# Kernel tuning notes

Measured on AMD Instinct MI355X. Metric: run time of the kernel, lower is better.

The kernel has to match this reference:

```python
import jax, jax.numpy as jnp
import numpy as np

S, B, D, H, F = 2048, 2, 1024, 16, 4096
HD = D // H
EPS = 1e-5


def setup_inputs() -> dict:
    key = jax.random.key(0)
    ks = jax.random.split(key, 16)
    sc_d = 1.0 / np.sqrt(D)
    sc_f = 1.0 / np.sqrt(F)
    return {
        "src": jax.random.normal(ks[0], (S, B, D), jnp.float32),
        # attention projections: Linear weights stored as [in, out] (y = x @ W + b)
        "Wq": jax.random.normal(ks[1], (D, D), jnp.float32) * sc_d,
        "bq": jnp.zeros((D,), jnp.float32),
        "Wk": jax.random.normal(ks[2], (D, D), jnp.float32) * sc_d,
        "bk": jnp.zeros((D,), jnp.float32),
        "Wv": jax.random.normal(ks[3], (D, D), jnp.float32) * sc_d,
        "bv": jnp.zeros((D,), jnp.float32),
        "Wo": jax.random.normal(ks[4], (D, D), jnp.float32) * sc_d,
        "bo": jnp.zeros((D,), jnp.float32),
        # norm1
        "g1": jnp.ones((D,), jnp.float32),
        "be1": jnp.zeros((D,), jnp.float32),
        # FFN
        "W1": jax.random.normal(ks[5], (D, F), jnp.float32) * sc_d,
        "bf1": jnp.zeros((F,), jnp.float32),
        "W2": jax.random.normal(ks[6], (F, D), jnp.float32) * sc_f,
        "bf2": jnp.zeros((D,), jnp.float32),
        # norm2
        "g2": jnp.ones((D,), jnp.float32),
        "be2": jnp.zeros((D,), jnp.float32),
    }


def _layernorm(x, g, b):
    m = jnp.mean(x, axis=-1, keepdims=True)
    v = jnp.mean(jnp.square(x - m), axis=-1, keepdims=True)
    return (x - m) * jax.lax.rsqrt(v + EPS) * g + b


def reference(src, Wq, bq, Wk, bk, Wv, bv, Wo, bo, g1, be1, W1, bf1, W2, bf2, g2, be2):
    # --- self attention (dropout_p=0 / eval mode => dropouts are identity) ---
    scaling = float(HD) ** -0.5
    q = (src @ Wq + bq) * scaling            # [S,B,D]
    k = src @ Wk + bk
    v = src @ Wv + bv
    # split heads: torch view(S, B*H, hd) == reshape(S, B, H, hd)
    qh = q.reshape(S, B, H, HD)
    kh = k.reshape(S, B, H, HD)
    vh = v.reshape(S, B, H, HD)
    scores = jnp.einsum("sbhd,tbhd->bhst", qh, kh)      # [B,H,S,S]
    attn = jax.nn.softmax(scores, axis=-1)
    ctx = jnp.einsum("bhst,tbhd->sbhd", attn, vh).reshape(S, B, D)
    attn_out = ctx @ Wo + bo
    # residual + norm1
    x = _layernorm(src + attn_out, g1, be1)
    # FFN (ReLU)
    ff = jax.nn.relu(x @ W1 + bf1) @ W2 + bf2
    # residual + norm2
    return _layernorm(x + ff, g2, be2)
```

## Files before the change

### kernel.cpp

```cpp
#include <hip/hip_runtime.h>
#include <hip/hip_bf16.h>

#define S_  2048
#define B_  2
#define D_  1024
#define H_  16
#define F_  4096
#define HD_ 64
#define NT_ (S_*B_)

typedef __attribute__((ext_vector_type(8))) short short8;
typedef __attribute__((ext_vector_type(4))) short short4v;
typedef __attribute__((ext_vector_type(4))) float f32x4;

#define MFMA16x16x32(a,b,c) __builtin_amdgcn_mfma_f32_16x16x32_bf16((a),(b),(c),0,0,0)

#define AS1C(p) ((const __attribute__((address_space(1))) void*)(p))
#define AS3(p)  ((__attribute__((address_space(3))) void*)(p))

__device__ __forceinline__ short f2b(float f) {
  union { float f; unsigned u; } x; x.f = f;
  unsigned r = x.u + 0x7FFFu + ((x.u >> 16) & 1u);
  return (short)(r >> 16);
}
__device__ __forceinline__ float b2f(short u) {
  union { unsigned u; float f; } x; x.u = ((unsigned)(unsigned short)u) << 16;
  return x.f;
}
__device__ __forceinline__ unsigned cvtpk(float a, float b) {
  unsigned r;
  asm("v_cvt_pk_bf16_f32 %0, %1, %2" : "=v"(r) : "v"(a), "v"(b));
  return r;
}
__device__ __forceinline__ float exp2fast(float x) {
  float r;
  asm("v_exp_f32 %0, %1" : "=v"(r) : "v"(x));
  return r;
}

__global__ __launch_bounds__(256) void prep_k(
    const float* __restrict__ src, short* __restrict__ xb,
    const float* __restrict__ Wq, const float* __restrict__ Wk,
    const float* __restrict__ Wv, const float* __restrict__ Wo,
    const float* __restrict__ W1, const float* __restrict__ W2,
    short* __restrict__ Wqkv_t, short* __restrict__ Wo_t,
    short* __restrict__ W1_t, short* __restrict__ W2_t) {
  __shared__ short t[32][33];
  int bid = blockIdx.x;
  if (bid < 2048) {
    int i = (bid * 256 + threadIdx.x) * 8;
    float4 a = *(const float4*)(src + i);
    float4 b = *(const float4*)(src + i + 4);
    short8 o;
    o[0] = f2b(a.x); o[1] = f2b(a.y); o[2] = f2b(a.z); o[3] = f2b(a.w);
    o[4] = f2b(b.x); o[5] = f2b(b.y); o[6] = f2b(b.z); o[7] = f2b(b.w);
    *(short8*)(xb + i) = o;
    return;
  }
  bid -= 2048;
  const float* W; short* Wt; int N, colbase, outK, bx, by;
  if (bid < 4096) {
    int which = bid >> 10, loc = bid & 1023;
    bx = loc & 31; by = loc >> 5;
    N = 1024; outK = 1024;
    if (which == 0)      { W = Wq; Wt = Wqkv_t; colbase = 0; }
    else if (which == 1) { W = Wk; Wt = Wqkv_t; colbase = 1024; }
    else if (which == 2) { W = Wv; Wt = Wqkv_t; colbase = 2048; }
    else                 { W = Wo; Wt = Wo_t;   colbase = 0; }
  } else if (bid < 8192) {
    int loc = bid - 4096;
    bx = loc & 127; by = loc >> 7;
    W = W1; Wt = W1_t; N = 4096; colbase = 0; outK = 1024;
  } else {
    int loc = bid - 8192;
    bx = loc & 31; by = loc >> 5;
    W = W2; Wt = W2_t; N = 1024; colbase = 0; outK = 4096;
  }
  int tx = threadIdx.x & 31, ty = threadIdx.x >> 5;
  int kbase = by * 32, nbase = bx * 32;
#pragma unroll
  for (int yy = 0; yy < 4; ++yy) {
    int kk = ty + yy * 8;
    t[kk][tx] = f2b(W[(size_t)(kbase + kk) * N + nbase + tx]);
  }
  __syncthreads();
#pragma unroll
  for (int yy = 0; yy < 4; ++yy) {
    int nn = ty + yy * 8;
    Wt[(size_t)(nbase + nn + colbase) * outK + kbase + tx] = t[tx][nn];
  }
}

template<int MODE>
__global__ __launch_bounds__(256, 2) void gemm_bt(
    const short* __restrict__ A, const short* __restrict__ Bt,
    int M, int N, int K, int lda,
    const float* __restrict__ bias0, const float* __restrict__ bias1,
    const float* __restrict__ bias2,
    float* __restrict__ outf,
    short* __restrict__ outq, short* __restrict__ outk, short* __restrict__ outv) {
  __shared__ __align__(16) short As[128 * 64];
  __shared__ __align__(16) short Bs[128 * 64];
  int tid = threadIdx.x;
  int lane = tid & 63, w = tid >> 6;
  int g = lane >> 4, r = lane & 15;
  int wm = w >> 1, wn = w & 1;

  int gx = gridDim.x, gy = gridDim.y;
  int nwg = gx * gy * gridDim.z;
  int flat = (blockIdx.z * gy + blockIdx.y) * gx + blockIdx.x;
  int cpx = nwg >> 3;
  int swz = (flat & 7) * cpx + (flat >> 3);
  int z = swz / (gx * gy);
  int rem = swz - z * gx * gy;
  int row0 = (rem / gx) * 128;
  int col0 = (rem % gx) * 128;
  size_t koff = (size_t)z * K;

  f32x4 acc[4][4];
#pragma unroll
  for (int m = 0; m < 4; ++m)
#pragma unroll
    for (int n = 0; n < 4; ++n) acc[m][n] = (f32x4){0.f, 0.f, 0.f, 0.f};

  for (int kt = 0; kt < K; kt += 64) {
#pragma unroll
    for (int p = 0; p < 4; ++p) {
      int idx = tid + p * 256;
      int row = idx >> 3, c = idx & 7;
      int scol = ((c ^ (row & 7)) << 3);
      __builtin_amdgcn_global_load_lds(AS1C(A  + (size_t)(row0 + row) * lda + koff + kt + scol),
                                       AS3(As + idx * 8), 16, 0, 0);
      __builtin_amdgcn_global_load_lds(AS1C(Bt + (size_t)(col0 + row) * lda + koff + kt + scol),
                                       AS3(Bs + idx * 8), 16, 0, 0);
    }
    __syncthreads();
    short8 af[4][2], bfr[4][2];
#pragma unroll
    for (int m = 0; m < 4; ++m)
#pragma unroll
      for (int kk = 0; kk < 2; ++kk) {
        int row = wm * 64 + m * 16 + r;
        af[m][kk] = *(const short8*)(As + row * 64 + (((kk * 4 + g) ^ (r & 7)) << 3));
      }
#pragma unroll
    for (int n = 0; n < 4; ++n)
#pragma unroll
      for (int kk = 0; kk < 2; ++kk) {
        int row = wn * 64 + n * 16 + r;
        bfr[n][kk] = *(const short8*)(Bs + row * 64 + (((kk * 4 + g) ^ (r & 7)) << 3));
      }
#pragma unroll
    for (int m = 0; m < 4; ++m)
#pragma unroll
      for (int n = 0; n < 4; ++n)
#pragma unroll
        for (int kk = 0; kk < 2; ++kk)
          acc[m][n] = MFMA16x16x32(af[m][kk], bfr[n][kk], acc[m][n]);
    __syncthreads();
  }

  int rb = row0 + wm * 64, cb = col0 + wn * 64;
#pragma unroll
  for (int m = 0; m < 4; ++m) {
#pragma unroll
    for (int n = 0; n < 4; ++n) {
#pragma unroll
      for (int j = 0; j < 4; ++j) {
        int row = rb + m * 16 + g * 4 + j;
        int col = cb + n * 16 + r;
        float v = acc[m][n][j];
        if (MODE == 0) {
          int s = row >> 1, b = row & 1;
          if (col < 1024) {
            float q = (v + bias0[col]) * (0.125f * 1.44269504088896f);
            int h = col >> 6, hd = col & 63;
            outq[((size_t)(b * H_ + h) * S_ + s) * HD_ + hd] = f2b(q);
          } else if (col < 2048) {
            int c2 = col - 1024;
            float kk = v + bias1[c2];
            int h = c2 >> 6, hd = c2 & 63;
            outk[((size_t)(b * H_ + h) * S_ + s) * HD_ + hd] = f2b(kk);
          } else {
            int c2 = col - 2048;
            float vv = v + bias2[c2];
            int h = c2 >> 6, hd = c2 & 63;
            outv[((size_t)(b * H_ + h) * HD_ + hd) * S_ + s] = f2b(vv);
          }
        } else if (MODE == 2) {
          size_t o = (size_t)row * N + col;
          float t = v + bias0[col];
          outq[o] = f2b(t > 0.f ? t : 0.f);
        } else {
          outf[(size_t)z * M * N + (size_t)row * N + col] = v;
        }
      }
    }
  }
}

__global__ __launch_bounds__(256, 4) void flash_attn(const short* __restrict__ Q,
                                                     const short* __restrict__ Kb,
                                                     const short* __restrict__ Vt,
                                                     short* __restrict__ ctx) {
  __shared__ __align__(16) short Ks[2][64 * 64];
  __shared__ __align__(16) short Vs[2][64 * 64];
  __shared__ __align__(16) short P[4][16][64];
  int tid = threadIdx.x;
  int lane = tid & 63, w = tid >> 6;
  int g = lane >> 4, r = lane & 15;
  int f = blockIdx.x;
  int xcd = f & 7, loc = f >> 3;
  int bh = xcd * 4 + (loc >> 5);
  int qt = loc & 31;
  const short* qp = Q  + (size_t)bh * S_ * HD_;
  const short* kp = Kb + (size_t)bh * S_ * HD_;
  const short* vp = Vt + (size_t)bh * HD_ * S_;
  int q0 = qt * 64 + w * 16;

  short8 qf[2];
#pragma unroll
  for (int kk = 0; kk < 2; ++kk)
    qf[kk] = *(const short8*)(qp + (size_t)(q0 + r) * HD_ + kk * 32 + g * 8);

  f32x4 acc[4];
  float mi = -1e30f, li = 0.f;
#pragma unroll
  for (int db = 0; db < 4; ++db) acc[db] = (f32x4){0.f, 0.f, 0.f, 0.f};

#pragma unroll
  for (int p = 0; p < 2; ++p) {
    int idx = tid + p * 256;
    int row = idx >> 3, c = idx & 7;
    int scol = ((c ^ (row & 7)) << 3);
    __builtin_amdgcn_global_load_lds(AS1C(kp + (size_t)row * HD_ + scol),
                                     AS3(&Ks[0][0] + idx * 8), 16, 0, 0);
    __builtin_amdgcn_global_load_lds(AS1C(vp + (size_t)row * S_ + scol),
                                     AS3(&Vs[0][0] + idx * 8), 16, 0, 0);
  }
  __syncthreads();

  int cur = 0;
  for (int t = 0; t < S_ / 64; ++t) {
    if (t + 1 < S_ / 64) {
      int kv1 = (t + 1) * 64;
#pragma unroll
      for (int p = 0; p < 2; ++p) {
        int idx = tid + p * 256;
        int row = idx >> 3, c = idx & 7;
        int scol = ((c ^ (row & 7)) << 3);
        __builtin_amdgcn_global_load_lds(AS1C(kp + (size_t)(kv1 + row) * HD_ + scol),
                                         AS3(&Ks[cur ^ 1][0] + idx * 8), 16, 0, 0);
        __builtin_amdgcn_global_load_lds(AS1C(vp + (size_t)row * S_ + kv1 + scol),
                                         AS3(&Vs[cur ^ 1][0] + idx * 8), 16, 0, 0);
      }
    }
    const short* Kc = &Ks[cur][0];
    const short* Vc = &Vs[cur][0];
    short8 kf[4][2];
#pragma unroll
    for (int kb = 0; kb < 4; ++kb)
#pragma unroll
      for (int kk = 0; kk < 2; ++kk) {
        int row = kb * 16 + r;
        kf[kb][kk] = *(const short8*)(Kc + row * 64 + (((kk * 4 + g) ^ (r & 7)) << 3));
      }

    f32x4 st[4];
    __builtin_amdgcn_s_setprio(1);
#pragma unroll
    for (int kb = 0; kb < 4; ++kb) {
      f32x4 tt = (f32x4){0.f, 0.f, 0.f, 0.f};
      tt = MFMA16x16x32(kf[kb][0], qf[0], tt);
      tt = MFMA16x16x32(kf[kb][1], qf[1], tt);
      st[kb] = tt;
    }
    __builtin_amdgcn_s_setprio(0);

    float t0 = fmaxf(fmaxf(st[0][0], st[0][1]), fmaxf(st[0][2], st[0][3]));
    float t1 = fmaxf(fmaxf(st[1][0], st[1][1]), fmaxf(st[1][2], st[1][3]));
    float t2 = fmaxf(fmaxf(st[2][0], st[2][1]), fmaxf(st[2][2], st[2][3]));
    float t3 = fmaxf(fmaxf(st[3][0], st[3][1]), fmaxf(st[3][2], st[3][3]));
    float pm = fmaxf(fmaxf(t0, t1), fmaxf(t2, t3));
    if (!__all(pm <= mi + 8.0f)) {
      pm = fmaxf(pm, __shfl_xor(pm, 16));
      pm = fmaxf(pm, __shfl_xor(pm, 32));
      float mn = fmaxf(mi, pm);
      float sc2 = exp2fast(mi - mn);
      mi = mn;
      li *= sc2;
#pragma unroll
      for (int db = 0; db < 4; ++db)
#pragma unroll
        for (int j = 0; j < 4; ++j) acc[db][j] *= sc2;
    }
    float rp[4];
#pragma unroll
    for (int kb = 0; kb < 4; ++kb) {
#pragma unroll
      for (int j = 0; j < 4; ++j) st[kb][j] = exp2fast(st[kb][j] - mi);
      rp[kb] = (st[kb][0] + st[kb][1]) + (st[kb][2] + st[kb][3]);
    }
    li += (rp[0] + rp[1]) + (rp[2] + rp[3]);

#pragma unroll
    for (int kb = 0; kb < 4; ++kb) {
      unsigned w0 = cvtpk(st[kb][0], st[kb][1]);
      unsigned w1 = cvtpk(st[kb][2], st[kb][3]);
      unsigned long long pw = (unsigned long long)w0 | ((unsigned long long)w1 << 32);
      int col = (kb * 16 + g * 4) ^ ((r & 7) << 3);
      *(unsigned long long*)(&P[w][r][0] + col) = pw;
    }

    short8 vf[4][2];
#pragma unroll
    for (int db = 0; db < 4; ++db)
#pragma unroll
      for (int ks = 0; ks < 2; ++ks) {
        int row = db * 16 + r;
        vf[db][ks] = *(const short8*)(Vc + row * 64 + (((ks * 4 + g) ^ (r & 7)) << 3));
      }
    short8 pf[2];
#pragma unroll
    for (int ks = 0; ks < 2; ++ks) {
      int col = (ks * 32 + g * 8) ^ ((r & 7) << 3);
      pf[ks] = *(const short8*)(&P[w][r][0] + col);
    }

    __builtin_amdgcn_s_setprio(1);
#pragma unroll
    for (int db = 0; db < 4; ++db) {
      acc[db] = MFMA16x16x32(vf[db][0], pf[0], acc[db]);
      acc[db] = MFMA16x16x32(vf[db][1], pf[1], acc[db]);
    }
    __builtin_amdgcn_s_setprio(0);

    __syncthreads();
    cur ^= 1;
  }

  li += __shfl_xor(li, 16);
  li += __shfl_xor(li, 32);

  int b = bh >> 4, h = bh & 15;
  float inv = 1.0f / li;
  int s = q0 + r;
  int token = s * B_ + b;
#pragma unroll
  for (int db = 0; db < 4; ++db) {
    unsigned w0 = cvtpk(acc[db][0] * inv, acc[db][1] * inv);
    unsigned w1 = cvtpk(acc[db][2] * inv, acc[db][3] * inv);
    unsigned long long pw = (unsigned long long)w0 | ((unsigned long long)w1 << 32);
    *(unsigned long long*)(ctx + (size_t)token * D_ + h * 64 + db * 16 + g * 4) = pw;
  }
}

template<int RESBF16, int WF, int WB>
__global__ __launch_bounds__(256) void layernorm_fused(
    const float* __restrict__ p0, const float* __restrict__ p1,
    const float* __restrict__ bias,
    const float* __restrict__ residf, const short* __restrict__ residb,
    const float* __restrict__ gm, const float* __restrict__ bt,
    float* __restrict__ of, short* __restrict__ ob) {
  __shared__ float r1[4], r2[4];
  int row = blockIdx.x, tid = threadIdx.x;
  size_t base = (size_t)row * D_ + tid * 4;
  float4 a = *(const float4*)(p0 + base);
  float4 b = *(const float4*)(p1 + base);
  float4 bi = *(const float4*)(bias + tid * 4);
  float4 v;
  if (RESBF16) {
    short4v rb = *(const short4v*)(residb + base);
    v.x = a.x + b.x + bi.x + b2f(rb[0]);
    v.y = a.y + b.y + bi.y + b2f(rb[1]);
    v.z = a.z + b.z + bi.z + b2f(rb[2]);
    v.w = a.w + b.w + bi.w + b2f(rb[3]);
  } else {
    float4 rf = *(const float4*)(residf + base);
    v.x = a.x + b.x + bi.x + rf.x;
    v.y = a.y + b.y + bi.y + rf.y;
    v.z = a.z + b.z + bi.z + rf.z;
    v.w = a.w + b.w + bi.w + rf.w;
  }
  float s1 = v.x + v.y + v.z + v.w;
  float s2 = v.x * v.x + v.y * v.y + v.z * v.z + v.w * v.w;
#pragma unroll
  for (int off = 32; off > 0; off >>= 1) {
    s1 += __shfl_xor(s1, off, 64);
    s2 += __shfl_xor(s2, off, 64);
  }
  int wid = tid >> 6;
  if ((tid & 63) == 0) { r1[wid] = s1; r2[wid] = s2; }
  __syncthreads();
  s1 = r1[0] + r1[1] + r1[2] + r1[3];
  s2 = r2[0] + r2[1] + r2[2] + r2[3];
  float mean = s1 * (1.0f / D_);
  float var = s2 * (1.0f / D_) - mean * mean;
  float rstd = rsqrtf(var + 1e-5f);
  float4 gv = *(const float4*)(gm + tid * 4);
  float4 bv = *(const float4*)(bt + tid * 4);
  float o0 = (v.x - mean) * rstd * gv.x + bv.x;
  float o1 = (v.y - mean) * rstd * gv.y + bv.y;
  float o2 = (v.z - mean) * rstd * gv.z + bv.z;
  float o3 = (v.w - mean) * rstd * gv.w + bv.w;
  if (WF) *(float4*)(of + base) = make_float4(o0, o1, o2, o3);
  if (WB) {
    short4v o;
    o[0] = f2b(o0); o[1] = f2b(o1); o[2] = f2b(o2); o[3] = f2b(o3);
    *(short4v*)(ob + base) = o;
  }
}

extern "C" void kernel_launch(void* const* d_in, const int* in_sizes, int n_in,
                              void* d_out, int out_size, void* d_ws, size_t ws_size,
                              hipStream_t stream) {
  const float* src = (const float*)d_in[0];
  const float* Wq  = (const float*)d_in[1];
  const float* bq  = (const float*)d_in[2];
  const float* Wk  = (const float*)d_in[3];
  const float* bk  = (const float*)d_in[4];
  const float* Wv  = (const float*)d_in[5];
  const float* bv  = (const float*)d_in[6];
  const float* Wo  = (const float*)d_in[7];
  const float* bo  = (const float*)d_in[8];
  const float* g1  = (const float*)d_in[9];
  const float* be1 = (const float*)d_in[10];
  const float* W1  = (const float*)d_in[11];
  const float* bf1 = (const float*)d_in[12];
  const float* W2  = (const float*)d_in[13];
  const float* bf2 = (const float*)d_in[14];
  const float* g2  = (const float*)d_in[15];
  const float* be2 = (const float*)d_in[16];
  float* out = (float*)d_out;
  char* ws = (char*)d_ws;

  const size_t MiB = 1024 * 1024;
  short* Wqkv_t = (short*)(ws + 0 * MiB);
  short* Wo_t   = (short*)(ws + 6 * MiB);
  short* W1_t   = (short*)(ws + 8 * MiB);
  short* W2_t   = (short*)(ws + 16 * MiB);
  short* xb     = (short*)(ws + 24 * MiB);
  short* x1b    = (short*)(ws + 24 * MiB);
  short* ctx    = (short*)(ws + 32 * MiB);
  short* qb_    = (short*)(ws + 40 * MiB);
  short* kb_    = (short*)(ws + 48 * MiB);
  short* vb_    = (short*)(ws + 56 * MiB);
  short* hid    = (short*)(ws + 32 * MiB);
  float* part   = (float*)(ws + 64 * MiB);
  float* part1  = part + (size_t)NT_ * D_;

  prep_k<<<14336, 256, 0, stream>>>(src, xb, Wq, Wk, Wv, Wo, W1, W2,
                                    Wqkv_t, Wo_t, W1_t, W2_t);

  gemm_bt<0><<<dim3(24, 32, 1), 256, 0, stream>>>(xb, Wqkv_t, NT_, 3072, 1024, 1024,
                                                  bq, bk, bv, nullptr, qb_, kb_, vb_);
  flash_attn<<<1024, 256, 0, stream>>>(qb_, kb_, vb_, ctx);
  gemm_bt<3><<<dim3(8, 32, 2), 256, 0, stream>>>(ctx, Wo_t, NT_, 1024, 512, 1024,
                                                 nullptr, nullptr, nullptr, part,
                                                 nullptr, nullptr, nullptr);
  layernorm_fused<0, 0, 1><<<NT_, 256, 0, stream>>>(part, part1, bo, src, nullptr,
                                                    g1, be1, nullptr, x1b);
  gemm_bt<2><<<dim3(32, 32, 1), 256, 0, stream>>>(x1b, W1_t, NT_, 4096, 1024, 1024,
                                                  bf1, nullptr, nullptr, nullptr,
                                                  hid, nullptr, nullptr);
  gemm_bt<3><<<dim3(8, 32, 2), 256, 0, stream>>>(hid, W2_t, NT_, 1024, 2048, 4096,
                                                 nullptr, nullptr, nullptr, part,
                                                 nullptr, nullptr, nullptr);
  layernorm_fused<1, 1, 0><<<NT_, 256, 0, stream>>>(part, part1, bf2, nullptr, x1b,
                                                    g2, be2, out, nullptr);
}
```

Measured before the change: 226.4 us.

## Give each flash-attention wave two query fragments and halve the block to 128 threads

The flash attention kernel now runs 2 waves per block instead of 4, and each wave handles 32 query rows as two 16-row fragments. Each K/V fragment read from shared memory then feeds twice as many MFMAs, which cuts LDS traffic per FLOP. Each thread also issues more of the global-to-LDS staging loads. The cost is roughly double the accumulator and score registers per wave, and fewer waves per block to hide latency, which may lower occupancy.

New measurement: 226.1 us. About the same (-0.1%).

```diff
diff --git a/kernel.cpp b/kernel.cpp
--- a/kernel.cpp
+++ b/kernel.cpp
@@ -199,13 +199,13 @@
   }
 }
 
-__global__ __launch_bounds__(256, 4) void flash_attn(const short* __restrict__ Q,
+__global__ __launch_bounds__(128, 2) void flash_attn(const short* __restrict__ Q,
                                                      const short* __restrict__ Kb,
                                                      const short* __restrict__ Vt,
                                                      short* __restrict__ ctx) {
   __shared__ __align__(16) short Ks[2][64 * 64];
   __shared__ __align__(16) short Vs[2][64 * 64];
-  __shared__ __align__(16) short P[4][16][64];
+  __shared__ __align__(16) short P[2][32][64];
   int tid = threadIdx.x;
   int lane = tid & 63, w = tid >> 6;
   int g = lane >> 4, r = lane & 15;
@@ -216,45 +216,45 @@
   const short* qp = Q  + (size_t)bh * S_ * HD_;
   const short* kp = Kb + (size_t)bh * S_ * HD_;
   const short* vp = Vt + (size_t)bh * HD_ * S_;
-  int q0 = qt * 64 + w * 16;
-
-  short8 qf[2];
-#pragma unroll
-  for (int kk = 0; kk < 2; ++kk)
-    qf[kk] = *(const short8*)(qp + (size_t)(q0 + r) * HD_ + kk * 32 + g * 8);
-
-  f32x4 acc[4];
-  float mi = -1e30f, li = 0.f;
-#pragma unroll
-  for (int db = 0; db < 4; ++db) acc[db] = (f32x4){0.f, 0.f, 0.f, 0.f};
-
-#pragma unroll
-  for (int p = 0; p < 2; ++p) {
-    int idx = tid + p * 256;
-    int row = idx >> 3, c = idx & 7;
-    int scol = ((c ^ (row & 7)) << 3);
-    __builtin_amdgcn_global_load_lds(AS1C(kp + (size_t)row * HD_ + scol),
-                                     AS3(&Ks[0][0] + idx * 8), 16, 0, 0);
-    __builtin_amdgcn_global_load_lds(AS1C(vp + (size_t)row * S_ + scol),
-                                     AS3(&Vs[0][0] + idx * 8), 16, 0, 0);
-  }
+  int q0 = qt * 64 + w * 32;
+
+  short8 qf[2][2];
+#pragma unroll
+  for (int fq = 0; fq < 2; ++fq)
+#pragma unroll
+    for (int kk = 0; kk < 2; ++kk)
+      qf[fq][kk] = *(const short8*)(qp + (size_t)(q0 + fq * 16 + r) * HD_ + kk * 32 + g * 8);
+
+  f32x4 acc[2][4];
+  float mi[2], li[2];
+#pragma unroll
+  for (int fq = 0; fq < 2; ++fq) {
+    mi[fq] = -1e30f; li[fq] = 0.f;
+#pragma unroll
+    for (int db = 0; db < 4; ++db) acc[fq][db] = (f32x4){0.f, 0.f, 0.f, 0.f};
+  }
+
+#define FA_STAGE(BUFK, BUFV, KOFF)                                                    \
+  {                                                                                   \
+    _Pragma("unroll")                                                                 \
+    for (int p = 0; p < 4; ++p) {                                                     \
+      int idx = tid + p * 128;                                                        \
+      int row = idx >> 3, c = idx & 7;                                                \
+      int scol = ((c ^ (row & 7)) << 3);                                              \
+      __builtin_amdgcn_global_load_lds(AS1C(kp + (size_t)((KOFF) + row) * HD_ + scol),\
+                                       AS3(BUFK + idx * 8), 16, 0, 0);                \
+      __builtin_amdgcn_global_load_lds(AS1C(vp + (size_t)row * S_ + (KOFF) + scol),   \
+                                       AS3(BUFV + idx * 8), 16, 0, 0);                \
+    }                                                                                 \
+  }
+
+  FA_STAGE(&Ks[0][0], &Vs[0][0], 0);
   __syncthreads();
 
   int cur = 0;
   for (int t = 0; t < S_ / 64; ++t) {
-    if (t + 1 < S_ / 64) {
-      int kv1 = (t + 1) * 64;
-#pragma unroll
-      for (int p = 0; p < 2; ++p) {
-        int idx = tid + p * 256;
-        int row = idx >> 3, c = idx & 7;
-        int scol = ((c ^ (row & 7)) << 3);
-        __builtin_amdgcn_global_load_lds(AS1C(kp + (size_t)(kv1 + row) * HD_ + scol),
-                                         AS3(&Ks[cur ^ 1][0] + idx * 8), 16, 0, 0);
-        __builtin_amdgcn_global_load_lds(AS1C(vp + (size_t)row * S_ + kv1 + scol),
-                                         AS3(&Vs[cur ^ 1][0] + idx * 8), 16, 0, 0);
-      }
-    }
+    if (t + 1 < S_ / 64) FA_STAGE(&Ks[cur ^ 1][0], &Vs[cur ^ 1][0], (t + 1) * 64);
+
     const short* Kc = &Ks[cur][0];
     const short* Vc = &Vs[cur][0];
     short8 kf[4][2];
@@ -266,50 +266,63 @@
         kf[kb][kk] = *(const short8*)(Kc + row * 64 + (((kk * 4 + g) ^ (r & 7)) << 3));
       }
 
-    f32x4 st[4];
+    f32x4 st[2][4];
     __builtin_amdgcn_s_setprio(1);
 #pragma unroll
-    for (int kb = 0; kb < 4; ++kb) {
-      f32x4 tt = (f32x4){0.f, 0.f, 0.f, 0.f};
-      tt = MFMA16x16x32(kf[kb][0], qf[0], tt);
-      tt = MFMA16x16x32(kf[kb][1], qf[1], tt);
-      st[kb] = tt;
-    }
+    for (int fq = 0; fq < 2; ++fq)
+#pragma unroll
+      for (int kb = 0; kb < 4; ++kb) {
+        f32x4 tt = (f32x4){0.f, 0.f, 0.f, 0.f};
+        tt = MFMA16x16x32(kf[kb][0], qf[fq][0], tt);
+        tt = MFMA16x16x32(kf[kb][1], qf[fq][1], tt);
+        st[fq][kb] = tt;
+      }
     __builtin_amdgcn_s_setprio(0);
 
-    float t0 = fmaxf(fmaxf(st[0][0], st[0][1]), fmaxf(st[0][2], st[0][3]));
-    float t1 = fmaxf(fmaxf(st[1][0], st[1][1]), fmaxf(st[1][2], st[1][3]));
-    float t2 = fmaxf(fmaxf(st[2][0], st[2][1]), fmaxf(st[2][2], st[2][3]));
-    float t3 = fmaxf(fmaxf(st[3][0], st[3][1]), fmaxf(st[3][2], st[3][3]));
-    float pm = fmaxf(fmaxf(t0, t1), fmaxf(t2, t3));
-    if (!__all(pm <= mi + 8.0f)) {
-      pm = fmaxf(pm, __shfl_xor(pm, 16));
-      pm = fmaxf(pm, __shfl_xor(pm, 32));
-      float mn = fmaxf(mi, pm);
-      float sc2 = exp2fast(mi - mn);
-      mi = mn;
-      li *= sc2;
-#pragma unroll
-      for (int db = 0; db < 4; ++db)
-#pragma unroll
-        for (int j = 0; j < 4; ++j) acc[db][j] *= sc2;
-    }
-    float rp[4];
-#pragma unroll
-    for (int kb = 0; kb < 4; ++kb) {
-#pragma unroll
-      for (int j = 0; j < 4; ++j) st[kb][j] = exp2fast(st[kb][j] - mi);
-      rp[kb] = (st[kb][0] + st[kb][1]) + (st[kb][2] + st[kb][3]);
-    }
-    li += (rp[0] + rp[1]) + (rp[2] + rp[3]);
-
-#pragma unroll
-    for (int kb = 0; kb < 4; ++kb) {
-      unsigned w0 = cvtpk(st[kb][0], st[kb][1]);
-      unsigned w1 = cvtpk(st[kb][2], st[kb][3]);
-      unsigned long long pw = (unsigned long long)w0 | ((unsigned long long)w1 << 32);
-      int col = (kb * 16 + g * 4) ^ ((r & 7) << 3);
-      *(unsigned long long*)(&P[w][r][0] + col) = pw;
+    float pm[2];
+#pragma unroll
+    for (int fq = 0; fq < 2; ++fq) {
+      float t0 = fmaxf(fmaxf(st[fq][0][0], st[fq][0][1]), fmaxf(st[fq][0][2], st[fq][0][3]));
+      float t1 = fmaxf(fmaxf(st[fq][1][0], st[fq][1][1]), fmaxf(st[fq][1][2], st[fq][1][3]));
+      float t2 = fmaxf(fmaxf(st[fq][2][0], st[fq][2][1]), fmaxf(st[fq][2][2], st[fq][2][3]));
+      float t3 = fmaxf(fmaxf(st[fq][3][0], st[fq][3][1]), fmaxf(st[fq][3][2], st[fq][3][3]));
+      pm[fq] = fmaxf(fmaxf(t0, t1), fmaxf(t2, t3));
+    }
+    if (!__all((pm[0] <= mi[0] + 8.0f) && (pm[1] <= mi[1] + 8.0f))) {
+#pragma unroll
+      for (int fq = 0; fq < 2; ++fq) {
+        float p = pm[fq];
+        p = fmaxf(p, __shfl_xor(p, 16));
+        p = fmaxf(p, __shfl_xor(p, 32));
+        float mn = fmaxf(mi[fq], p);
+        float sc2 = exp2fast(mi[fq] - mn);
+        mi[fq] = mn;
+        li[fq] *= sc2;
+#pragma unroll
+        for (int db = 0; db < 4; ++db)
+#pragma unroll
+          for (int j = 0; j < 4; ++j) acc[fq][db][j] *= sc2;
+      }
+    }
+#pragma unroll
+    for (int fq = 0; fq < 2; ++fq) {
+      float rp[4];
+#pragma unroll
+      for (int kb = 0; kb < 4; ++kb) {
+#pragma unroll
+        for (int j = 0; j < 4; ++j) st[fq][kb][j] = exp2fast(st[fq][kb][j] - mi[fq]);
+        rp[kb] = (st[fq][kb][0] + st[fq][kb][1]) + (st[fq][kb][2] + st[fq][kb][3]);
+      }
+      li[fq] += (rp[0] + rp[1]) + (rp[2] + rp[3]);
+
+#pragma unroll
+      for (int kb = 0; kb < 4; ++kb) {
+        unsigned w0 = cvtpk(st[fq][kb][0], st[fq][kb][1]);
+        unsigned w1 = cvtpk(st[fq][kb][2], st[fq][kb][3]);
+        unsigned long long pw = (unsigned long long)w0 | ((unsigned long long)w1 << 32);
+        int col = (kb * 16 + g * 4) ^ ((r & 7) << 3);
+        *(unsigned long long*)(&P[w][fq * 16 + r][0] + col) = pw;
+      }
     }
 
     short8 vf[4][2];
@@ -320,38 +333,46 @@
         int row = db * 16 + r;
         vf[db][ks] = *(const short8*)(Vc + row * 64 + (((ks * 4 + g) ^ (r & 7)) << 3));
       }
-    short8 pf[2];
-#pragma unroll
-    for (int ks = 0; ks < 2; ++ks) {
-      int col = (ks * 32 + g * 8) ^ ((r & 7) << 3);
-      pf[ks] = *(const short8*)(&P[w][r][0] + col);
-    }
+    short8 pf[2][2];
+#pragma unroll
+    for (int fq = 0; fq < 2; ++fq)
+#pragma unroll
+      for (int ks = 0; ks < 2; ++ks) {
+        int col = (ks * 32 + g * 8) ^ ((r & 7) << 3);
+        pf[fq][ks] = *(const short8*)(&P[w][fq * 16 + r][0] + col);
+      }
 
     __builtin_amdgcn_s_setprio(1);
 #pragma unroll
-    for (int db = 0; db < 4; ++db) {
-      acc[db] = MFMA16x16x32(vf[db][0], pf[0], acc[db]);
-      acc[db] = MFMA16x16x32(vf[db][1], pf[1], acc[db]);
-    }
+    for (int fq = 0; fq < 2; ++fq)
+#pragma unroll
+      for (int db = 0; db < 4; ++db) {
+        acc[fq][db] = MFMA16x16x32(vf[db][0], pf[fq][0], acc[fq][db]);
+        acc[fq][db] = MFMA16x16x32(vf[db][1], pf[fq][1], acc[fq][db]);
+      }
     __builtin_amdgcn_s_setprio(0);
 
     __syncthreads();
     cur ^= 1;
   }
-
-  li += __shfl_xor(li, 16);
-  li += __shfl_xor(li, 32);
+#undef FA_STAGE
 
   int b = bh >> 4, h = bh & 15;
-  float inv = 1.0f / li;
-  int s = q0 + r;
-  int token = s * B_ + b;
-#pragma unroll
-  for (int db = 0; db < 4; ++db) {
-    unsigned w0 = cvtpk(acc[db][0] * inv, acc[db][1] * inv);
-    unsigned w1 = cvtpk(acc[db][2] * inv, acc[db][3] * inv);
-    unsigned long long pw = (unsigned long long)w0 | ((unsigned long long)w1 << 32);
-    *(unsigned long long*)(ctx + (size_t)token * D_ + h * 64 + db * 16 + g * 4) = pw;
+#pragma unroll
+  for (int fq = 0; fq < 2; ++fq) {
+    float l = li[fq];
+    l += __shfl_xor(l, 16);
+    l += __shfl_xor(l, 32);
+    float inv = 1.0f / l;
+    int s = q0 + fq * 16 + r;
+    int token = s * B_ + b;
+#pragma unroll
+    for (int db = 0; db < 4; ++db) {
+      unsigned w0 = cvtpk(acc[fq][db][0] * inv, acc[fq][db][1] * inv);
+      unsigned w1 = cvtpk(acc[fq][db][2] * inv, acc[fq][db][3] * inv);
+      unsigned long long pw = (unsigned long long)w0 | ((unsigned long long)w1 << 32);
+      *(unsigned long long*)(ctx + (size_t)token * D_ + h * 64 + db * 16 + g * 4) = pw;
+    }
   }
 }
 
@@ -454,7 +475,7 @@
 
   gemm_bt<0><<<dim3(24, 32, 1), 256, 0, stream>>>(xb, Wqkv_t, NT_, 3072, 1024, 1024,
                                                   bq, bk, bv, nullptr, qb_, kb_, vb_);
-  flash_attn<<<1024, 256, 0, stream>>>(qb_, kb_, vb_, ctx);
+  flash_attn<<<1024, 128, 0, stream>>>(qb_, kb_, vb_, ctx);
   gemm_bt<3><<<dim3(8, 32, 2), 256, 0, stream>>>(ctx, Wo_t, NT_, 1024, 512, 1024,
                                                  nullptr, nullptr, nullptr, part,
                                                  nullptr, nullptr, nullptr);
```
